# Performance work log

Measured on AMD Instinct MI355X. Metric: run time of the kernel, lower is better.

The kernel has to match this reference:

```python
import jax, jax.numpy as jnp
import numpy as np

N_NODES = 100000
N_RAND_EDGES = 1600000
EPS = 1e-12


def setup_inputs() -> dict:
    key = jax.random.key(0)
    k_x, k_w1, k_w2, k_r, k_c = jax.random.split(key, 5)
    X = jax.random.normal(k_x, (N_NODES, 256), dtype=jnp.float32)
    # Linear weights stored as [in, out] so forward is X @ W (bias=False)
    W1 = jax.random.normal(k_w1, (256, 128), dtype=jnp.float32) * 0.05
    W2 = jax.random.normal(k_w2, (128, 64), dtype=jnp.float32) * 0.05
    row = jax.random.randint(k_r, (N_RAND_EDGES,), 0, N_NODES, dtype=jnp.int32)
    col = jax.random.randint(k_c, (N_RAND_EDGES,), 0, N_NODES, dtype=jnp.int32)
    loops = jnp.arange(N_NODES, dtype=jnp.int32)  # self-loops (A has self-loops)
    edge_row = jnp.concatenate([row, loops])
    edge_col = jnp.concatenate([col, loops])
    return {"X": X, "W1": W1, "W2": W2, "edge_row": edge_row, "edge_col": edge_col}


def _norm_edge_weights(edge_row, edge_col):
    # degrees = row-sums of A (all values are 1.0)
    deg = jax.ops.segment_sum(jnp.ones_like(edge_row, dtype=jnp.float32), edge_row,
                              num_segments=N_NODES)
    d_inv_sqrt = 1.0 / jnp.clip(jnp.sqrt(deg), EPS)
    # A_hat = D^-1/2 A D^-1/2  <=>  per-edge weight
    return d_inv_sqrt[edge_row] * d_inv_sqrt[edge_col]


def _spmm(w, edge_row, edge_col, X):
    # (A_hat @ X)[i] = sum_{e: row_e = i} w_e * X[col_e]
    return jax.ops.segment_sum(w[:, None] * X[edge_col], edge_row,
                               num_segments=N_NODES)


def reference(X, W1, W2, edge_row, edge_col):
    w = _norm_edge_weights(edge_row, edge_col)
    # layer 0: GraphConvolution -> ReLU (dropout is identity in eval mode)
    H = jax.nn.relu(_spmm(w, edge_row, edge_col, X @ W1))
    # layer 1: GraphConvolution (logits)
    out = _spmm(w, edge_row, edge_col, H @ W2)
    return out
```

## Files before the change

### kernel.cpp

```cpp
#include <hip/hip_runtime.h>
#include <hip/hip_bf16.h>


typedef __attribute__((ext_vector_type(8))) short short8;
typedef __attribute__((ext_vector_type(4))) float floatx4;
typedef __attribute__((ext_vector_type(2))) float floatx2;

static __device__ __forceinline__ ushort f32_to_bf16_bits(float f) {
    union { ushort u; __hip_bfloat16 b; } cv;
    cv.b = __float2bfloat16(f);
    return cv.u;
}
static __device__ __forceinline__ float bf16lo_to_f32(uint u) {
    return __uint_as_float(u << 16);
}
static __device__ __forceinline__ float bf16hi_to_f32(uint u) {
    return __uint_as_float(u & 0xffff0000u);
}
static __device__ __forceinline__ uint pack2bf(float a, float b) {
    return (uint)f32_to_bf16_bits(a) | ((uint)f32_to_bf16_bits(b) << 16);
}

#define CSR_EPB 8192
#define SPMM_CHUNK 1024

__global__ __launch_bounds__(256) void scan_phase1_kernel(
    const int* __restrict__ in, int* __restrict__ out,
    int* __restrict__ block_total, int n) {
    __shared__ int tsum[256];
    int t = threadIdx.x;
    int base = blockIdx.x * 1024 + t * 4;
    int v0 = (base + 0 < n) ? in[base + 0] : 0;
    int v1 = (base + 1 < n) ? in[base + 1] : 0;
    int v2 = (base + 2 < n) ? in[base + 2] : 0;
    int v3 = (base + 3 < n) ? in[base + 3] : 0;
    tsum[t] = v0 + v1 + v2 + v3;
    __syncthreads();
    for (int off = 1; off < 256; off <<= 1) {
        int x = (t >= off) ? tsum[t - off] : 0;
        __syncthreads();
        tsum[t] += x;
        __syncthreads();
    }
    if (t == 255) block_total[blockIdx.x] = tsum[255];
    int run = (t == 0) ? 0 : tsum[t - 1];
    if (base + 0 < n) out[base + 0] = run; run += v0;
    if (base + 1 < n) out[base + 1] = run; run += v1;
    if (base + 2 < n) out[base + 2] = run; run += v2;
    if (base + 3 < n) out[base + 3] = run;
}

__global__ __launch_bounds__(256) void scan_phase2_kernel(
    const int* __restrict__ block_total, int* __restrict__ block_offset, int G) {
    __shared__ int s[256];
    int t = threadIdx.x;
    s[t] = (t < G) ? block_total[t] : 0;
    __syncthreads();
    for (int off = 1; off < 256; off <<= 1) {
        int x = (t >= off) ? s[t - off] : 0;
        __syncthreads();
        s[t] += x;
        __syncthreads();
    }
    if (t < G) block_offset[t] = (t == 0) ? 0 : s[t - 1];
    if (t == 0) block_offset[G] = s[255];
}

__global__ __launch_bounds__(256) void scan_phase3_kernel(
    int* __restrict__ arr, const int* __restrict__ block_offset, int n, int G) {
    int i = blockIdx.x * blockDim.x + threadIdx.x;
    if (i < n) arr[i] += block_offset[i >> 10];
    if (i == 0) arr[n] = block_offset[G];
}

__global__ __launch_bounds__(256) void edge_hist_cast_kernel(
    const int* __restrict__ keys, int* __restrict__ histG, int E, int nblk,
    const float* __restrict__ W1, const float* __restrict__ W2,
    ushort* __restrict__ W1t, ushort* __restrict__ W2t) {
    int b = blockIdx.x;
    if (b >= nblk) {
        int i = (b - nblk) * 256 + threadIdx.x;
        if (i < 256 * 128) {
            int n = i >> 8, k = i & 255;
            W1t[i] = f32_to_bf16_bits(W1[k * 128 + n]);
        } else {
            int j = i - 256 * 128;
            if (j < 128 * 64) {
                int n = j >> 7, k = j & 127;
                W2t[j] = f32_to_bf16_bits(W2[k * 64 + n]);
            }
        }
        return;
    }
    __shared__ int h[256];
    int t = threadIdx.x;
    h[t] = 0;
    __syncthreads();
    int base = b * CSR_EPB;
    int end = min(base + CSR_EPB, E);
    for (int i = base + t; i < end; i += 256)
        atomicAdd(&h[keys[i] >> 9], 1);
    __syncthreads();
    histG[t * nblk + b] = h[t];
}

__global__ __launch_bounds__(256) void edge_bin_kernel(
    const int* __restrict__ rows, const int* __restrict__ colsIn,
    const int* __restrict__ offG, const int* __restrict__ blk_off1,
    int* __restrict__ binP, int E, int nblk) {
    __shared__ int cur[256];
    int t = threadIdx.x;
    int idx = t * nblk + blockIdx.x;
    cur[t] = offG[idx] + blk_off1[idx >> 10];
    __syncthreads();
    int base = blockIdx.x * CSR_EPB;
    int end = min(base + CSR_EPB, E);
    for (int i = base + t; i < end; i += 256) {
        int r = rows[i], c = colsIn[i];
        int p = atomicAdd(&cur[r >> 9], 1);
        binP[p] = ((r & 511) << 17) | c;
    }
}

__global__ __launch_bounds__(256) void deg_dinv_from_bin_kernel(
    const int* __restrict__ binP, const int* __restrict__ offG,
    const int* __restrict__ blk_off1,
    int* __restrict__ deg, float* __restrict__ dinv, int E, int nblk, int N) {
    __shared__ int cnt[512];
    int b = blockIdx.x;
    int rbase = b << 9;
    if (rbase >= N) return;
    int t = threadIdx.x;
    for (int i = t; i < 512; i += 256) cnt[i] = 0;
    __syncthreads();
    int i0 = b * nblk;
    int bs = offG[i0] + blk_off1[i0 >> 10];
    int be = E;
    if (b + 1 < 256) {
        int i1 = (b + 1) * nblk;
        be = offG[i1] + blk_off1[i1 >> 10];
    }
    for (int e = bs + t; e < be; e += 256)
        atomicAdd(&cnt[binP[e] >> 17], 1);
    __syncthreads();
    for (int i = t; i < 512; i += 256) {
        int r = rbase + i;
        if (r < N) {
            int d = cnt[i];
            deg[r] = d;
            dinv[r] = 1.0f / sqrtf(fmaxf((float)d, 1e-24f));
        }
    }
}

__global__ __launch_bounds__(256) void edge_scatter_kernel(
    const int* __restrict__ binP, const int* __restrict__ offG,
    const int* __restrict__ blk_off1,
    const int* __restrict__ row_ptr, int* __restrict__ csr_col,
    int E, int nblk, int N) {
    __shared__ int cur[512];
    int b = blockIdx.x;
    int rbase = b << 9;
    if (rbase >= N) return;
    int t = threadIdx.x;
    for (int i = t; i < 512; i += 256) {
        int r = rbase + i;
        cur[i] = (r < N) ? row_ptr[r] : 0;
    }
    __syncthreads();
    int i0 = b * nblk;
    int bs = offG[i0] + blk_off1[i0 >> 10];
    int be = E;
    if (b + 1 < 256) {
        int i1 = (b + 1) * nblk;
        be = offG[i1] + blk_off1[i1 >> 10];
    }
    for (int e = bs + t; e < be; e += 256) {
        int pk = binP[e];
        int rl = pk >> 17;
        int c = pk & 0x1ffff;
        int p = atomicAdd(&cur[rl], 1);
        csr_col[p] = c;
    }
}

template <int KTOT, int NCOLS, bool AF32>
__global__ __launch_bounds__(256) void gemm_mfma_kernel(
    const void* __restrict__ Aptr, const ushort* __restrict__ Bt,
    const float* __restrict__ dinv, ushort* __restrict__ Cbf, int M) {
    constexpr int KP = 128;
    constexpr int COLT = NCOLS / 16;
    __shared__ ushort Bs[NCOLS][KP + 8];
    int tid = threadIdx.x;
    int wave = tid >> 6, lane = tid & 63;
    int quad = lane >> 4, l16 = lane & 15;
    int row0 = blockIdx.x * 64;
    int rowA = row0 + wave * 16 + l16;
    int rowAc = min(rowA, M - 1);

    floatx4 acc[COLT];
#pragma unroll
    for (int t = 0; t < COLT; t++) acc[t] = (floatx4){0.f, 0.f, 0.f, 0.f};

    for (int kp = 0; kp < KTOT; kp += KP) {
        for (int u = tid; u < NCOLS * (KP / 8); u += 256) {
            int n = u / (KP / 8);
            int k8 = (u % (KP / 8)) * 8;
            *(short8*)&Bs[n][k8] = *(const short8*)(Bt + (size_t)n * KTOT + kp + k8);
        }
        __syncthreads();
#pragma unroll
        for (int kc = 0; kc < KP / 32; kc++) {
            int kk = kp + kc * 32 + quad * 8;
            short8 a;
            if (AF32) {
                const float* ap = (const float*)Aptr + (size_t)rowAc * KTOT + kk;
#pragma unroll
                for (int j = 0; j < 8; j++) a[j] = (short)f32_to_bf16_bits(ap[j]);
            } else {
                a = *(const short8*)((const ushort*)Aptr + (size_t)rowAc * KTOT + kk);
            }
#pragma unroll
            for (int t = 0; t < COLT; t++) {
                short8 b = *(const short8*)&Bs[t * 16 + l16][kc * 32 + quad * 8];
                acc[t] = __builtin_amdgcn_mfma_f32_16x16x32_bf16(a, b, acc[t], 0, 0, 0);
            }
        }
        __syncthreads();
    }

#pragma unroll
    for (int r = 0; r < 4; r++) {
        int row = row0 + wave * 16 + quad * 4 + r;
        if (row < M) {
            float dv = dinv[row];
#pragma unroll
            for (int t = 0; t < COLT; t++)
                Cbf[(size_t)row * NCOLS + t * 16 + l16] = f32_to_bf16_bits(dv * acc[t][r]);
        }
    }
}

__global__ __launch_bounds__(256) void spmm_gemm2_kernel(
    const int* __restrict__ row_ptr, const int* __restrict__ cols,
    const float* __restrict__ dinv, const ushort* __restrict__ XW1,
    const ushort* __restrict__ W2t, ushort* __restrict__ HW2, int n) {
    __shared__ int cstage[SPMM_CHUNK];
    __shared__ ushort W2s[64][136];
    __shared__ ushort Hs[16][136];

    int tid = threadIdx.x;
    int wv = tid >> 6;
    int lane = tid & 63;
    int g = lane >> 4, lg = lane & 15;
    int r0 = blockIdx.x * 16;
    int row = r0 + wv * 4 + g;
    bool ok = row < n;
    int rc = ok ? row : (n - 1);
    int beg = row_ptr[rc];
    int end = ok ? row_ptr[rc + 1] : beg;
    int bbeg = row_ptr[r0];
    int bend = row_ptr[min(r0 + 16, n)];

    for (int u = tid; u < 64 * 16; u += 256) {
        int nn = u >> 4, k8 = (u & 15) * 8;
        *(short8*)&W2s[nn][k8] = *(const short8*)(W2t + nn * 128 + k8);
    }

    floatx2 acc2[4];
#pragma unroll
    for (int i = 0; i < 4; i++) acc2[i] = (floatx2){0.f, 0.f};

    const ushort* xb = XW1 + lg * 8;

#define ACC_DW(U, D)                                            \
    {                                                            \
        floatx2 v_;                                              \
        v_.x = bf16lo_to_f32(U);                                 \
        v_.y = bf16hi_to_f32(U);                                 \
        acc2[D] += v_;                                           \
    }
#define ACC_U4(UU)                                               \
    ACC_DW(UU.x, 0) ACC_DW(UU.y, 1) ACC_DW(UU.z, 2) ACC_DW(UU.w, 3)

    for (int cb = bbeg; cb < bend; cb += SPMM_CHUNK) {
        int ce = min(cb + SPMM_CHUNK, bend);
        __syncthreads();
        for (int i = cb + tid; i < ce; i += 256)
            cstage[i - cb] = cols[i];
        __syncthreads();
        int s = max(beg, cb), t_ = min(end, ce);
        int e = s;
        for (; e + 8 <= t_; e += 8) {
            int c0 = cstage[e - cb], c1 = cstage[e + 1 - cb];
            int c2 = cstage[e + 2 - cb], c3 = cstage[e + 3 - cb];
            int c4 = cstage[e + 4 - cb], c5 = cstage[e + 5 - cb];
            int c6 = cstage[e + 6 - cb], c7 = cstage[e + 7 - cb];
            uint4 u0 = *(const uint4*)(xb + (size_t)c0 * 128);
            uint4 u1 = *(const uint4*)(xb + (size_t)c1 * 128);
            uint4 u2 = *(const uint4*)(xb + (size_t)c2 * 128);
            uint4 u3 = *(const uint4*)(xb + (size_t)c3 * 128);
            uint4 u4 = *(const uint4*)(xb + (size_t)c4 * 128);
            uint4 u5 = *(const uint4*)(xb + (size_t)c5 * 128);
            uint4 u6 = *(const uint4*)(xb + (size_t)c6 * 128);
            uint4 u7 = *(const uint4*)(xb + (size_t)c7 * 128);
            ACC_U4(u0) ACC_U4(u1) ACC_U4(u2) ACC_U4(u3)
            ACC_U4(u4) ACC_U4(u5) ACC_U4(u6) ACC_U4(u7)
        }
        for (; e + 4 <= t_; e += 4) {
            int c0 = cstage[e - cb], c1 = cstage[e + 1 - cb];
            int c2 = cstage[e + 2 - cb], c3 = cstage[e + 3 - cb];
            uint4 u0 = *(const uint4*)(xb + (size_t)c0 * 128);
            uint4 u1 = *(const uint4*)(xb + (size_t)c1 * 128);
            uint4 u2 = *(const uint4*)(xb + (size_t)c2 * 128);
            uint4 u3 = *(const uint4*)(xb + (size_t)c3 * 128);
            ACC_U4(u0) ACC_U4(u1) ACC_U4(u2) ACC_U4(u3)
        }
        for (; e < t_; e++) {
            int c = cstage[e - cb];
            uint4 u = *(const uint4*)(xb + (size_t)c * 128);
            ACC_U4(u)
        }
    }
#undef ACC_U4
#undef ACC_DW

    {
        float dv = ok ? dinv[row] : 0.f;
        float a0 = fmaxf(dv * acc2[0].x, 0.f), a1 = fmaxf(dv * acc2[0].y, 0.f);
        float a2 = fmaxf(dv * acc2[1].x, 0.f), a3 = fmaxf(dv * acc2[1].y, 0.f);
        float a4 = fmaxf(dv * acc2[2].x, 0.f), a5 = fmaxf(dv * acc2[2].y, 0.f);
        float a6 = fmaxf(dv * acc2[3].x, 0.f), a7 = fmaxf(dv * acc2[3].y, 0.f);
        uint4 o;
        o.x = pack2bf(a0, a1);
        o.y = pack2bf(a2, a3);
        o.z = pack2bf(a4, a5);
        o.w = pack2bf(a6, a7);
        *(uint4*)&Hs[wv * 4 + g][lg * 8] = o;
    }
    __syncthreads();

    int quad = g, l16 = lg;
    floatx4 dacc = (floatx4){0.f, 0.f, 0.f, 0.f};
#pragma unroll
    for (int kc = 0; kc < 4; kc++) {
        short8 a = *(const short8*)&Hs[l16][kc * 32 + quad * 8];
        short8 b = *(const short8*)&W2s[wv * 16 + l16][kc * 32 + quad * 8];
        dacc = __builtin_amdgcn_mfma_f32_16x16x32_bf16(a, b, dacc, 0, 0, 0);
    }
#pragma unroll
    for (int r = 0; r < 4; r++) {
        int rowD = r0 + quad * 4 + r;
        if (rowD < n)
            HW2[(size_t)rowD * 64 + wv * 16 + l16] =
                f32_to_bf16_bits(dinv[rowD] * dacc[r]);
    }
}

__global__ __launch_bounds__(256) void spmm_f64_kernel(
    const int* __restrict__ row_ptr, const int* __restrict__ cols,
    const float* __restrict__ dinv, const ushort* __restrict__ Xin,
    float* __restrict__ Yout, int n) {
    __shared__ int cstage[SPMM_CHUNK];
    int r0 = blockIdx.x * 16;
    int tid = threadIdx.x;
    int wv = tid >> 6;
    int lane = tid & 63;
    int g = lane >> 4, lg = lane & 15;
    int row = r0 + wv * 4 + g;
    bool ok = row < n;
    int rc = ok ? row : (n - 1);
    int beg = row_ptr[rc];
    int end = ok ? row_ptr[rc + 1] : beg;
    int bbeg = row_ptr[r0];
    int bend = row_ptr[min(r0 + 16, n)];

    floatx2 acc2[2];
    acc2[0] = (floatx2){0.f, 0.f};
    acc2[1] = (floatx2){0.f, 0.f};

    const ushort* xb = Xin + lg * 4;

#define ACC_DW(U, D)                                            \
    {                                                            \
        floatx2 v_;                                              \
        v_.x = bf16lo_to_f32(U);                                 \
        v_.y = bf16hi_to_f32(U);                                 \
        acc2[D] += v_;                                           \
    }
#define ACC_U2(UU) ACC_DW(UU.x, 0) ACC_DW(UU.y, 1)

    for (int cb = bbeg; cb < bend; cb += SPMM_CHUNK) {
        int ce = min(cb + SPMM_CHUNK, bend);
        __syncthreads();
        for (int i = cb + tid; i < ce; i += 256)
            cstage[i - cb] = cols[i];
        __syncthreads();
        int s = max(beg, cb), t_ = min(end, ce);
        int e = s;
        for (; e + 8 <= t_; e += 8) {
            int c0 = cstage[e - cb], c1 = cstage[e + 1 - cb];
            int c2 = cstage[e + 2 - cb], c3 = cstage[e + 3 - cb];
            int c4 = cstage[e + 4 - cb], c5 = cstage[e + 5 - cb];
            int c6 = cstage[e + 6 - cb], c7 = cstage[e + 7 - cb];
            uint2 u0 = *(const uint2*)(xb + (size_t)c0 * 64);
            uint2 u1 = *(const uint2*)(xb + (size_t)c1 * 64);
            uint2 u2 = *(const uint2*)(xb + (size_t)c2 * 64);
            uint2 u3 = *(const uint2*)(xb + (size_t)c3 * 64);
            uint2 u4 = *(const uint2*)(xb + (size_t)c4 * 64);
            uint2 u5 = *(const uint2*)(xb + (size_t)c5 * 64);
            uint2 u6 = *(const uint2*)(xb + (size_t)c6 * 64);
            uint2 u7 = *(const uint2*)(xb + (size_t)c7 * 64);
            ACC_U2(u0) ACC_U2(u1) ACC_U2(u2) ACC_U2(u3)
            ACC_U2(u4) ACC_U2(u5) ACC_U2(u6) ACC_U2(u7)
        }
        for (; e + 4 <= t_; e += 4) {
            int c0 = cstage[e - cb], c1 = cstage[e + 1 - cb];
            int c2 = cstage[e + 2 - cb], c3 = cstage[e + 3 - cb];
            uint2 u0 = *(const uint2*)(xb + (size_t)c0 * 64);
            uint2 u1 = *(const uint2*)(xb + (size_t)c1 * 64);
            uint2 u2 = *(const uint2*)(xb + (size_t)c2 * 64);
            uint2 u3 = *(const uint2*)(xb + (size_t)c3 * 64);
            ACC_U2(u0) ACC_U2(u1) ACC_U2(u2) ACC_U2(u3)
        }
        for (; e < t_; e++) {
            int c = cstage[e - cb];
            uint2 u = *(const uint2*)(xb + (size_t)c * 64);
            ACC_U2(u)
        }
    }
#undef ACC_U2
#undef ACC_DW

    if (ok) {
        float dv = dinv[row];
        float4 o = make_float4(dv * acc2[0].x, dv * acc2[0].y,
                               dv * acc2[1].x, dv * acc2[1].y);
        *(float4*)(Yout + (size_t)row * 64 + lg * 4) = o;
    }
}


extern "C" void kernel_launch(void* const* d_in, const int* in_sizes, int n_in,
                              void* d_out, int out_size, void* d_ws, size_t ws_size,
                              hipStream_t stream) {
    const float* X  = (const float*)d_in[0];
    const float* W1 = (const float*)d_in[1];
    const float* W2 = (const float*)d_in[2];
    const int* erow = (const int*)d_in[3];
    const int* ecol = (const int*)d_in[4];

    const int N = in_sizes[0] / 256;
    const int E = in_sizes[3];
    const int G = (N + 1023) >> 10;

    const int nblk = (E + CSR_EPB - 1) / CSR_EPB;
    const int SL = 256 * nblk;
    const int GS = (SL + 1023) >> 10;
    const int GMAX = (G > GS) ? G : GS;
    const int CAST_BLKS = (256 * 128 + 128 * 64 + 255) / 256;

    char* ws = (char*)d_ws;
    size_t off = 0;
    auto carve = [&](size_t bytes) -> char* {
        char* p = ws + off;
        off += (bytes + 255) & ~(size_t)255;
        return p;
    };
    int*    deg       = (int*)   carve((size_t)N * 4);
    float*  dinv      = (float*) carve((size_t)N * 4);
    int*    row_ptr   = (int*)   carve((size_t)(N + 1) * 4);
    int*    blk_total = (int*)   carve((size_t)GMAX * 4);
    int*    blk_off1  = (int*)   carve((size_t)(GMAX + 1) * 4);
    int*    blk_off2  = (int*)   carve((size_t)(GMAX + 1) * 4);
    int*    offG      = (int*)   carve((size_t)(SL + 1) * 4);
    size_t binP_bytes = (size_t)E * 4;
    size_t xw1_bytes  = (size_t)N * 128 * 2;
    char*  uni        = carve(binP_bytes > xw1_bytes ? binP_bytes : xw1_bytes);
    int*    binP      = (int*)uni;
    ushort* XW1       = (ushort*)uni;
    int*    csr_col   = (int*)   carve((size_t)E * 4);
    ushort* W1t       = (ushort*)carve((size_t)256 * 128 * 2);
    ushort* W2t       = (ushort*)carve((size_t)128 * 64 * 2);
    ushort* HW2       = (ushort*)carve((size_t)N * 64 * 2);

    edge_hist_cast_kernel<<<nblk + CAST_BLKS, 256, 0, stream>>>(
        erow, offG, E, nblk, W1, W2, W1t, W2t);
    scan_phase1_kernel<<<GS, 256, 0, stream>>>(offG, offG, blk_total, SL);
    scan_phase2_kernel<<<1, 256, 0, stream>>>(blk_total, blk_off1, GS);
    edge_bin_kernel<<<nblk, 256, 0, stream>>>(erow, ecol, offG, blk_off1, binP, E, nblk);

    deg_dinv_from_bin_kernel<<<256, 256, 0, stream>>>(binP, offG, blk_off1, deg, dinv, E, nblk, N);
    scan_phase1_kernel<<<G, 256, 0, stream>>>(deg, row_ptr, blk_total, N);
    scan_phase2_kernel<<<1, 256, 0, stream>>>(blk_total, blk_off2, G);
    scan_phase3_kernel<<<(N + 255) / 256, 256, 0, stream>>>(row_ptr, blk_off2, N, G);

    edge_scatter_kernel<<<256, 256, 0, stream>>>(binP, offG, blk_off1, row_ptr, csr_col, E, nblk, N);

    gemm_mfma_kernel<256, 128, true><<<(N + 63) / 64, 256, 0, stream>>>(
        (const void*)X, W1t, dinv, XW1, N);

    spmm_gemm2_kernel<<<(N + 15) / 16, 256, 0, stream>>>(
        row_ptr, csr_col, dinv, XW1, W2t, HW2, N);

    spmm_f64_kernel<<<(N + 15) / 16, 256, 0, stream>>>(row_ptr, csr_col, dinv, HW2, (float*)d_out, N);
}
```

Measured before the change: 348.2 us.

## Split final SpMM by feature halves, vectorize fp32 A loads, drop W2 LDS staging

The final SpMM now gives each block 32 rows and one 32-column half of the 64 features. Block IDs are interleaved so the two halves of the same row group are scheduled close together and can share cached gathers. The GEMM's fp32 A-operand load becomes two float4 loads instead of eight scalar loads. The fused SpMM+GEMM2 kernel reads W2 fragments straight from global memory into registers instead of staging them in LDS, which cuts LDS use and may help occupancy. The cost is that each edge's column index is now read by two blocks, and W2 is read redundantly from cache by every block.

```diff
diff --git a/kernel.cpp b/kernel.cpp
--- a/kernel.cpp
+++ b/kernel.cpp
@@ -215,8 +215,16 @@
             short8 a;
             if (AF32) {
                 const float* ap = (const float*)Aptr + (size_t)rowAc * KTOT + kk;
-#pragma unroll
-                for (int j = 0; j < 8; j++) a[j] = (short)f32_to_bf16_bits(ap[j]);
+                float4 f0 = *(const float4*)ap;
+                float4 f1 = *(const float4*)(ap + 4);
+                a[0] = (short)f32_to_bf16_bits(f0.x);
+                a[1] = (short)f32_to_bf16_bits(f0.y);
+                a[2] = (short)f32_to_bf16_bits(f0.z);
+                a[3] = (short)f32_to_bf16_bits(f0.w);
+                a[4] = (short)f32_to_bf16_bits(f1.x);
+                a[5] = (short)f32_to_bf16_bits(f1.y);
+                a[6] = (short)f32_to_bf16_bits(f1.z);
+                a[7] = (short)f32_to_bf16_bits(f1.w);
             } else {
                 a = *(const short8*)((const ushort*)Aptr + (size_t)rowAc * KTOT + kk);
             }
@@ -246,7 +254,6 @@
     const float* __restrict__ dinv, const ushort* __restrict__ XW1,
     const ushort* __restrict__ W2t, ushort* __restrict__ HW2, int n) {
     __shared__ int cstage[SPMM_CHUNK];
-    __shared__ ushort W2s[64][136];
     __shared__ ushort Hs[16][136];
 
     int tid = threadIdx.x;
@@ -261,11 +268,6 @@
     int end = ok ? row_ptr[rc + 1] : beg;
     int bbeg = row_ptr[r0];
     int bend = row_ptr[min(r0 + 16, n)];
-
-    for (int u = tid; u < 64 * 16; u += 256) {
-        int nn = u >> 4, k8 = (u & 15) * 8;
-        *(short8*)&W2s[nn][k8] = *(const short8*)(W2t + nn * 128 + k8);
-    }
 
     floatx2 acc2[4];
 #pragma unroll
@@ -340,19 +342,21 @@
     }
     __syncthreads();
 
-    int quad = g, l16 = lg;
+    short8 bf[4];
+#pragma unroll
+    for (int kc = 0; kc < 4; kc++)
+        bf[kc] = *(const short8*)(W2t + (wv * 16 + lg) * 128 + kc * 32 + g * 8);
     floatx4 dacc = (floatx4){0.f, 0.f, 0.f, 0.f};
 #pragma unroll
     for (int kc = 0; kc < 4; kc++) {
-        short8 a = *(const short8*)&Hs[l16][kc * 32 + quad * 8];
-        short8 b = *(const short8*)&W2s[wv * 16 + l16][kc * 32 + quad * 8];
-        dacc = __builtin_amdgcn_mfma_f32_16x16x32_bf16(a, b, dacc, 0, 0, 0);
+        short8 a = *(const short8*)&Hs[lg][kc * 32 + g * 8];
+        dacc = __builtin_amdgcn_mfma_f32_16x16x32_bf16(a, bf[kc], dacc, 0, 0, 0);
     }
 #pragma unroll
     for (int r = 0; r < 4; r++) {
-        int rowD = r0 + quad * 4 + r;
+        int rowD = r0 + g * 4 + r;
         if (rowD < n)
-            HW2[(size_t)rowD * 64 + wv * 16 + l16] =
+            HW2[(size_t)rowD * 64 + wv * 16 + lg] =
                 f32_to_bf16_bits(dinv[rowD] * dacc[r]);
     }
 }
@@ -360,26 +364,33 @@
 __global__ __launch_bounds__(256) void spmm_f64_kernel(
     const int* __restrict__ row_ptr, const int* __restrict__ cols,
     const float* __restrict__ dinv, const ushort* __restrict__ Xin,
-    float* __restrict__ Yout, int n) {
+    float* __restrict__ Yout, int n, int RB) {
     __shared__ int cstage[SPMM_CHUNK];
-    int r0 = blockIdx.x * 16;
+    int bid = blockIdx.x;
+    int rb8 = bid >> 3;
+    int sub = bid & 7;
+    int fh = sub >> 2;
+    int rowblk = rb8 * 4 + (sub & 3);
+    if (rowblk >= RB) return;
+    int r0 = rowblk * 32;
+
     int tid = threadIdx.x;
     int wv = tid >> 6;
     int lane = tid & 63;
-    int g = lane >> 4, lg = lane & 15;
-    int row = r0 + wv * 4 + g;
+    int h = lane >> 3, lh = lane & 7;
+    int row = r0 + wv * 8 + h;
     bool ok = row < n;
     int rc = ok ? row : (n - 1);
     int beg = row_ptr[rc];
     int end = ok ? row_ptr[rc + 1] : beg;
     int bbeg = row_ptr[r0];
-    int bend = row_ptr[min(r0 + 16, n)];
+    int bend = row_ptr[min(r0 + 32, n)];
 
     floatx2 acc2[2];
     acc2[0] = (floatx2){0.f, 0.f};
     acc2[1] = (floatx2){0.f, 0.f};
 
-    const ushort* xb = Xin + lg * 4;
+    const ushort* xb = Xin + fh * 32 + lh * 4;
 
 #define ACC_DW(U, D)                                            \
     {                                                            \
@@ -414,15 +425,6 @@
             ACC_U2(u0) ACC_U2(u1) ACC_U2(u2) ACC_U2(u3)
             ACC_U2(u4) ACC_U2(u5) ACC_U2(u6) ACC_U2(u7)
         }
-        for (; e + 4 <= t_; e += 4) {
-            int c0 = cstage[e - cb], c1 = cstage[e + 1 - cb];
-            int c2 = cstage[e + 2 - cb], c3 = cstage[e + 3 - cb];
-            uint2 u0 = *(const uint2*)(xb + (size_t)c0 * 64);
-            uint2 u1 = *(const uint2*)(xb + (size_t)c1 * 64);
-            uint2 u2 = *(const uint2*)(xb + (size_t)c2 * 64);
-            uint2 u3 = *(const uint2*)(xb + (size_t)c3 * 64);
-            ACC_U2(u0) ACC_U2(u1) ACC_U2(u2) ACC_U2(u3)
-        }
         for (; e < t_; e++) {
             int c = cstage[e - cb];
             uint2 u = *(const uint2*)(xb + (size_t)c * 64);
@@ -436,7 +438,7 @@
         float dv = dinv[row];
         float4 o = make_float4(dv * acc2[0].x, dv * acc2[0].y,
                                dv * acc2[1].x, dv * acc2[1].y);
-        *(float4*)(Yout + (size_t)row * 64 + lg * 4) = o;
+        *(float4*)(Yout + (size_t)row * 64 + fh * 32 + lh * 4) = o;
     }
 }
 
@@ -503,5 +505,8 @@
     spmm_gemm2_kernel<<<(N + 15) / 16, 256, 0, stream>>>(
         row_ptr, csr_col, dinv, XW1, W2t, HW2, N);
 
-    spmm_f64_kernel<<<(N + 15) / 16, 256, 0, stream>>>(row_ptr, csr_col, dinv, HW2, (float*)d_out, N);
-}
+    const int RB = (N + 31) / 32;
+    const int F64_BLKS = ((RB + 3) / 4) * 8;
+    spmm_f64_kernel<<<F64_BLKS, 256, 0, stream>>>(
+        row_ptr, csr_col, dinv, HW2, (float*)d_out, N, RB);
+}
```

New measurement: 369.2 us. 6.0% more time.
